# Optimization experiments

Hardware: AMD Instinct MI355X
Metric: run time of the kernel (lower is better)

## Reference

```python
import jax, jax.numpy as jnp
import numpy as np

N, E, MUL, ATTR, NBASIS = 30000, 480000, 32, 8, 8
AVG_NEIGH = 16.0
INV_SQRT3 = 1.0 / np.sqrt(3.0).astype(np.float32)  # wigner 3j (1,1,0)
LOG2 = float(np.log(2.0))


def ssp(x):
    # shifted softplus: softplus(x) - log(2)
    return jax.nn.softplus(x) - LOG2


def setup_inputs() -> dict:
    key = jax.random.key(0)
    ks = jax.random.split(key, 15)
    return {
        "node_s": jax.random.normal(ks[0], (N, MUL), jnp.float32),
        "node_v": jax.random.normal(ks[1], (N, MUL, 3), jnp.float32),
        "node_attr": jax.random.uniform(ks[2], (N, ATTR), jnp.float32),
        "edge_attr": jax.random.normal(ks[3], (E, 4), jnp.float32),       # [sh0 | sh1(3)]
        "edge_scalars": jax.random.uniform(ks[4], (E, NBASIS), jnp.float32),
        "W1_0": jax.random.normal(ks[5], (MUL, MUL), jnp.float32),
        "W1_1": jax.random.normal(ks[6], (MUL, MUL), jnp.float32),
        "Wfc1": jax.random.normal(ks[7], (NBASIS, NBASIS), jnp.float32),
        "Wfc2": jax.random.normal(ks[8], (NBASIS, 4 * MUL), jnp.float32),
        "W2_0": jax.random.normal(ks[9], (2 * MUL, MUL), jnp.float32),
        "W2_1": jax.random.normal(ks[10], (2 * MUL, MUL), jnp.float32),
        "Wsc0": jax.random.normal(ks[11], (MUL, ATTR, MUL), jnp.float32),
        "Wsc1": jax.random.normal(ks[12], (MUL, ATTR, MUL), jnp.float32),
        "edge_src": jax.random.randint(ks[13], (E,), 0, N, jnp.int32),
        "edge_dst": jax.random.randint(ks[14], (E,), 0, N, jnp.int32),
    }


def reference(node_s, node_v, node_attr, edge_attr, edge_scalars,
              W1_0, W1_1, Wfc1, Wfc2, W2_0, W2_1, Wsc0, Wsc1,
              edge_src, edge_dst):
    n_nodes, mul = node_s.shape
    # --- fc: radial MLP -> per-edge TP weights (shared_weights=False) ---
    h = ssp(edge_scalars @ Wfc1 * (1.0 / np.sqrt(Wfc1.shape[0])))
    w = h @ Wfc2 * (1.0 / np.sqrt(Wfc2.shape[0]))                 # [E, 4*MUL]
    w00, w01, w10, w11 = jnp.split(w, 4, axis=1)                  # instruction order
    # --- lin1: per-irrep linear (fan-in normalized) ---
    inv_m = 1.0 / np.sqrt(mul)
    x0 = node_s @ W1_0 * inv_m                                    # [N, MUL]
    x1 = jnp.einsum('nud,uw->nwd', node_v, W1_1) * inv_m          # [N, MUL, 3]
    # --- gather destination-node features per edge ---
    x0d, x1d = x0[edge_dst], x1[edge_dst]
    sh0, sh1 = edge_attr[:, :1], edge_attr[:, 1:4]
    # --- uvu tensor product with per-edge weights ---
    s_a = w00 * x0d * sh0                                         # 0e x 0e -> 0e
    s_b = w11 * jnp.einsum('eud,ed->eu', x1d, sh1) * INV_SQRT3    # 1o x 1o -> 0e
    v_a = (w01 * x0d)[:, :, None] * sh1[:, None, :]               # 0e x 1o -> 1o
    v_b = w10[:, :, None] * x1d * sh0[:, :, None]                 # 1o x 0e -> 1o
    mid_s = jnp.concatenate([s_a, s_b], axis=1)                   # [E, 64]  (64x0e)
    mid_v = jnp.concatenate([v_a, v_b], axis=1)                   # [E, 64, 3] (64x1o)
    # --- scatter-sum over edge_src, normalized by sqrt(avg_num_neighbors) ---
    inv_nb = 1.0 / np.sqrt(AVG_NEIGH)
    agg_s = jax.ops.segment_sum(mid_s, edge_src, num_segments=n_nodes) * inv_nb
    agg_v = jax.ops.segment_sum(mid_v, edge_src, num_segments=n_nodes) * inv_nb
    # --- lin2 ---
    inv_2m = 1.0 / np.sqrt(2.0 * mul)
    out0 = agg_s @ W2_0 * inv_2m                                  # [N, MUL]
    out1 = jnp.einsum('nud,uw->nwd', agg_v, W2_1) * inv_2m        # [N, MUL, 3]
    # --- self-connection: fully-connected TP (attr is scalar 8x0e) ---
    sc_norm = 1.0 / np.sqrt(mul * node_attr.shape[1])
    sc0 = jnp.einsum('nu,nv,uvw->nw', node_s, node_attr, Wsc0) * sc_norm
    sc1 = jnp.einsum('nud,nv,uvw->nwd', node_v, node_attr, Wsc1) * sc_norm
    o0 = out0 + sc0
    o1 = out1 + sc1
    return jnp.concatenate([o0, o1.reshape(n_nodes, mul * 3)], axis=1)  # [N, 128]
```

## Files before the change

### kernel.cpp

```cpp
#include <hip/hip_runtime.h>
#include <math.h>

#define N_NODES 30000
#define N_EDGES 480000

typedef __attribute__((ext_vector_type(8))) short short8;
typedef __attribute__((ext_vector_type(4))) float f32x4;
typedef __attribute__((ext_vector_type(2))) float f32x2;

__device__ __forceinline__ unsigned short f2bf(float f) {
    unsigned u = __float_as_uint(f);
    u += 0x7fff + ((u >> 16) & 1);
    return (unsigned short)(u >> 16);
}
__device__ __forceinline__ float bfLO(unsigned v) { return __uint_as_float(v << 16); }
__device__ __forceinline__ float bfHI(unsigned v) { return __uint_as_float(v & 0xffff0000u); }
__device__ __forceinline__ unsigned packbf(float a, float b) {
    return (unsigned)f2bf(a) | ((unsigned)f2bf(b) << 16);
}
__device__ __forceinline__ unsigned ptk(float a, float b) {
    return (__float_as_uint(a) >> 16) | (__float_as_uint(b) & 0xffff0000u);
}

union U8 { short8 v; unsigned u[4]; };
union C4 { f32x4 v; float f[4]; };

__global__ __launch_bounds__(256) void k_pre(
    const float* __restrict__ node_s,
    const float* __restrict__ node_v,
    const float* __restrict__ W1_0,
    const float* __restrict__ W1_1,
    const float* __restrict__ Wsc0,
    const float* __restrict__ Wsc1,
    const float* __restrict__ W2_0,
    const float* __restrict__ W2_1,
    const int* __restrict__ edge_src,
    int* __restrict__ deg,
    unsigned short* __restrict__ xnode,
    unsigned* __restrict__ bsc0,
    unsigned* __restrict__ bsc1,
    unsigned* __restrict__ b20,
    unsigned* __restrict__ b21)
{
    __shared__ float sVT[16 * 100];
    __shared__ float sXo[16 * 140];
    int tid = threadIdx.x;

    if (blockIdx.x >= 1875) {
        int b = blockIdx.x - 1875;
        const float* Wm = (b == 0) ? Wsc0 : (b == 1) ? Wsc1 : (b == 2) ? W2_0 : W2_1;
        unsigned* dst = (b == 0) ? bsc0 : (b == 1) ? bsc1 : (b == 2) ? b20 : b21;
        float scale = (b < 2) ? 0.0625f : 0.03125f;
        int nu = (b < 2) ? 4096 : 1024;
        for (int idx = tid; idx < nu; idx += 256) {
            int jp = idx & 3;
            int lane = (idx >> 2) & 63;
            int ft = (idx >> 8) & 1;
            int kc = idx >> 9;
            int quad = lane >> 4, col = lane & 15;
            int k = kc * 32 + quad * 8 + jp * 2;
            int c = ft * 16 + col;
            dst[idx] = packbf(Wm[k * 32 + c] * scale, Wm[(k + 1) * 32 + c] * scale);
        }
        return;
    }

    atomicAdd(&deg[edge_src[blockIdx.x * 256 + tid]], 1);

    int nbase = blockIdx.x * 16;
    for (int i = tid; i < 1536; i += 256) {
        int nl = i / 96, r = i - nl * 96;
        int u = r / 3, d = r - u * 3;
        sVT[nl * 100 + d * 32 + u] = node_v[(size_t)nbase * 96 + i];
    }
    __syncthreads();

    int lane = tid & 63;
    int wv = tid >> 6;
    int col = lane & 15, quad = lane >> 4, m = lane & 15;

    const float* W1 = (wv == 0) ? W1_0 : W1_1;
    U8 bf0, bf1;
#pragma unroll
    for (int p = 0; p < 4; ++p) {
        int k = quad * 8 + 2 * p;
        bf0.u[p] = packbf(W1[k * 32 + col],      W1[(k + 1) * 32 + col]);
        bf1.u[p] = packbf(W1[k * 32 + col + 16], W1[(k + 1) * 32 + col + 16]);
    }

    U8 af;
    if (wv == 0) {
        const float* sp = node_s + (size_t)(nbase + m) * 32 + quad * 8;
        float4 a0 = *(const float4*)(sp);
        float4 a1 = *(const float4*)(sp + 4);
        af.u[0] = packbf(a0.x, a0.y); af.u[1] = packbf(a0.z, a0.w);
        af.u[2] = packbf(a1.x, a1.y); af.u[3] = packbf(a1.z, a1.w);
    } else {
        int R = 16 * (wv - 1) + m;
        int nl = R / 3, d = R - nl * 3;
        const float* vp = sVT + nl * 100 + d * 32 + quad * 8;
        af.u[0] = packbf(vp[0], vp[1]); af.u[1] = packbf(vp[2], vp[3]);
        af.u[2] = packbf(vp[4], vp[5]); af.u[3] = packbf(vp[6], vp[7]);
    }

    f32x4 acc0 = {0.f, 0.f, 0.f, 0.f};
    f32x4 acc1 = {0.f, 0.f, 0.f, 0.f};
    acc0 = __builtin_amdgcn_mfma_f32_16x16x32_bf16(af.v, bf0.v, acc0, 0, 0, 0);
    acc1 = __builtin_amdgcn_mfma_f32_16x16x32_bf16(af.v, bf1.v, acc1, 0, 0, 0);

    C4 c0, c1;
    c0.v = acc0; c1.v = acc1;
    if (wv == 0) {
#pragma unroll
        for (int r = 0; r < 4; ++r) {
            int nl = (quad << 2) + r;
            sXo[nl * 140 + col]      = c0.f[r];
            sXo[nl * 140 + col + 16] = c1.f[r];
        }
    } else {
#pragma unroll
        for (int r = 0; r < 4; ++r) {
            int R = 16 * (wv - 1) + (quad << 2) + r;
            int nl = R / 3, d = R - nl * 3;
            sXo[nl * 140 + (1 + d) * 34 + col]      = c0.f[r];
            sXo[nl * 140 + (1 + d) * 34 + col + 16] = c1.f[r];
        }
    }
    __syncthreads();

    const float inv_m = 0.1767766953f;
    for (int i = tid; i < 512; i += 256) {
        int nl = i >> 5, u = i & 31;
        const float* xp = sXo + nl * 140;
        uint2 pk;
        pk.x = packbf(xp[u] * inv_m,       xp[34 + u] * inv_m);
        pk.y = packbf(xp[68 + u] * inv_m,  xp[102 + u] * inv_m);
        *(uint2*)(xnode + (size_t)(nbase + nl) * 128 + u * 4) = pk;
    }
}

__global__ __launch_bounds__(1024) void scan_kernel(const int* __restrict__ deg,
                                                    int* __restrict__ offs,
                                                    int* __restrict__ cursor) {
    __shared__ int sdeg[N_NODES];
    __shared__ int wsum[16];
    int tid = threadIdx.x;
#pragma unroll
    for (int k = 0; k < 30; ++k) {
        int idx = k * 1024 + tid;
        if (idx < N_NODES) sdeg[idx] = deg[idx];
    }
    __syncthreads();
    int base = tid * 30;
    int s = 0;
    if (base < N_NODES) {
#pragma unroll
        for (int k = 0; k < 30; ++k) s += sdeg[base + k];
    }
    int lane = tid & 63, wid = tid >> 6;
    int inc = s;
#pragma unroll
    for (int d = 1; d < 64; d <<= 1) {
        int o = __shfl_up(inc, d, 64);
        if (lane >= d) inc += o;
    }
    if (lane == 63) wsum[wid] = inc;
    __syncthreads();
    if (tid < 16) {
        int v = wsum[tid];
        int t = v;
#pragma unroll
        for (int d = 1; d < 16; d <<= 1) {
            int o = __shfl_up(t, d, 64);
            if (tid >= d) t += o;
        }
        wsum[tid] = t - v;
    }
    __syncthreads();
    int run = inc - s + wsum[wid];
    if (base < N_NODES) {
#pragma unroll
        for (int k = 0; k < 30; ++k) {
            int n = base + k;
            int d = sdeg[n];
            sdeg[n] = run;
            run += d;
        }
    }
    __syncthreads();
#pragma unroll
    for (int k = 0; k < 30; ++k) {
        int idx = k * 1024 + tid;
        if (idx < N_NODES) {
            int v = sdeg[idx];
            offs[idx] = v;
            cursor[idx] = v;
        }
    }
    if (tid == 0) offs[N_NODES] = N_EDGES;
}

__global__ __launch_bounds__(256) void fill_kernel(
    const float* __restrict__ edge_attr,
    const float* __restrict__ edge_scalars,
    const float* __restrict__ Wfc1,
    const int* __restrict__ edge_src,
    const int* __restrict__ edge_dst,
    int* __restrict__ cursor,
    uint4* __restrict__ rec)
{
    __shared__ float sW[64];
    int tid = threadIdx.x;
    if (tid < 64) sW[tid] = Wfc1[tid];
    __syncthreads();

    int e = blockIdx.x * 256 + tid;
    float4 es0 = *(const float4*)(edge_scalars + (size_t)e * 8);
    float4 es1 = *(const float4*)(edge_scalars + (size_t)e * 8 + 4);
    float4 ea  = *(const float4*)(edge_attr + (size_t)e * 4);
    int src = edge_src[e];
    int dst = edge_dst[e];
    int pos = atomicAdd(&cursor[src], 1);

    const float inv8 = 0.3535533906f;
    float h[8];
#pragma unroll
    for (int i = 0; i < 8; ++i) {
        float acc = es0.x * sW[0 * 8 + i];
        acc = fmaf(es0.y, sW[1 * 8 + i], acc);
        acc = fmaf(es0.z, sW[2 * 8 + i], acc);
        acc = fmaf(es0.w, sW[3 * 8 + i], acc);
        acc = fmaf(es1.x, sW[4 * 8 + i], acc);
        acc = fmaf(es1.y, sW[5 * 8 + i], acc);
        acc = fmaf(es1.z, sW[6 * 8 + i], acc);
        acc = fmaf(es1.w, sW[7 * 8 + i], acc);
        acc *= inv8;
        float ax = fabsf(acc);
        float tt = __expf(-ax);
        h[i] = fmaxf(acc, 0.f) + __logf(1.f + tt) - 0.6931471806f;
    }
    uint4 r0, r1;
    r0.x = packbf(h[0], h[1]); r0.y = packbf(h[2], h[3]);
    r0.z = packbf(h[4], h[5]); r0.w = packbf(h[6], h[7]);
    r1.x = packbf(ea.x, ea.y); r1.y = packbf(ea.z, ea.w);
    r1.z = (unsigned)dst; r1.w = 0;
    rec[2 * pos]     = r0;
    rec[2 * pos + 1] = r1;
}

__global__ __launch_bounds__(256) void k_main(
    const int* __restrict__ offs,
    const uint4* __restrict__ rec,
    const float* __restrict__ Wfc2,
    const unsigned short* __restrict__ xnode,
    const float* __restrict__ node_s,
    const float* __restrict__ node_v,
    const float* __restrict__ node_attr,
    const unsigned* __restrict__ bsc0,
    const unsigned* __restrict__ bsc1,
    const unsigned* __restrict__ b20,
    const unsigned* __restrict__ b21,
    float* __restrict__ out)
{
    __shared__ float sS[16 * 33];
    __shared__ float sV[16 * 100];
    __shared__ unsigned short sAgg[16 * 264];
    int tid = threadIdx.x;
    int lane = tid & 63;
    int u = lane & 31;
    int half = lane >> 5;
    int wv = tid >> 6;
    int nbase = blockIdx.x * 16;

    for (int i = tid; i < 512; i += 256)
        sS[(i >> 5) * 33 + (i & 31)] = node_s[(size_t)nbase * 32 + i];
    for (int i = tid; i < 1536; i += 256)
        sV[(i / 96) * 100 + (i % 96)] = node_v[(size_t)nbase * 96 + i];

    const float inv8 = 0.3535533906f;
    const float inv_s3 = 0.5773502692f;
    f32x2 wfA[8], wfB[8];
#pragma unroll
    for (int i = 0; i < 8; ++i) {
        wfA[i].x = Wfc2[i * 128 + u] * inv8;
        wfA[i].y = Wfc2[i * 128 + 32 + u] * inv8;
        wfB[i].x = Wfc2[i * 128 + 64 + u] * inv8;
        wfB[i].y = Wfc2[i * 128 + 96 + u] * inv8 * inv_s3;
    }

    for (int jn = 0; jn < 4; ++jn) {
        int nl = wv * 4 + jn;
        int node = nbase + nl;
        int beg = offs[node], end = offs[node + 1];
        float a_sa = 0.f, a_sb = 0.f;
        f32x2 a_va01 = {0.f, 0.f}, a_vb01 = {0.f, 0.f};
        float a_va2 = 0.f, a_vb2 = 0.f;

        if (end > beg) {
            int last = end - 1;
            int i = beg + half;
            int p = min(i, last);
            uint4 a0 = rec[2 * p], a1 = rec[2 * p + 1];
            p = min(i + 2, last);
            uint4 b0 = rec[2 * p], b1 = rec[2 * p + 1];
            p = min(i + 4, last);
            uint4 c0 = rec[2 * p], c1 = rec[2 * p + 1];
            uint2 xA = *(const uint2*)(xnode + (size_t)(int)a1.z * 128 + u * 4);
            uint2 xB = *(const uint2*)(xnode + (size_t)(int)b1.z * 128 + u * 4);

            for (; i < end; i += 2) {
                int pD = min(i + 6, last);
                uint4 d0 = rec[2 * pD], d1 = rec[2 * pD + 1];
                uint2 xC = *(const uint2*)(xnode + (size_t)(int)c1.z * 128 + u * 4);

                float hv[8];
                hv[0] = bfLO(a0.x); hv[1] = bfHI(a0.x);
                hv[2] = bfLO(a0.y); hv[3] = bfHI(a0.y);
                hv[4] = bfLO(a0.z); hv[5] = bfHI(a0.z);
                hv[6] = bfLO(a0.w); hv[7] = bfHI(a0.w);
                f32x2 aA = {0.f, 0.f}, aB = {0.f, 0.f};
#pragma unroll
                for (int q = 0; q < 8; ++q) {
                    f32x2 hh = {hv[q], hv[q]};
                    aA = __builtin_elementwise_fma(hh, wfA[q], aA);
                    aB = __builtin_elementwise_fma(hh, wfB[q], aB);
                }
                float a00 = aA.x, a01 = aA.y, a10 = aB.x, a11 = aB.y;

                float sh0 = bfLO(a1.x), s1xe = bfHI(a1.x);
                float s1ye = bfLO(a1.y), s1ze = bfHI(a1.y);
                float x0 = bfLO(xA.x), xd0 = bfHI(xA.x);
                float xd1 = bfLO(xA.y), xd2 = bfHI(xA.y);

                float dot = xd0 * s1xe + xd1 * s1ye + xd2 * s1ze;
                a_sa = fmaf(a00 * sh0, x0, a_sa);
                a_sb = fmaf(a11, dot, a_sb);
                float w01x0 = a01 * x0;
                float t10 = a10 * sh0;
                f32x2 wb = {w01x0, w01x0};
                f32x2 tb = {t10, t10};
                f32x2 s01 = {s1xe, s1ye};
                f32x2 xd01 = {xd0, xd1};
                a_va01 = __builtin_elementwise_fma(wb, s01, a_va01);
                a_vb01 = __builtin_elementwise_fma(tb, xd01, a_vb01);
                a_va2 = fmaf(w01x0, s1ze, a_va2);
                a_vb2 = fmaf(t10, xd2, a_vb2);

                a0 = b0; a1 = b1; xA = xB;
                b0 = c0; b1 = c1; xB = xC;
                c0 = d0; c1 = d1;
            }
        }
        a_sa    += __shfl_xor(a_sa, 32, 64);
        a_sb    += __shfl_xor(a_sb, 32, 64);
        a_va01.x += __shfl_xor(a_va01.x, 32, 64);
        a_va01.y += __shfl_xor(a_va01.y, 32, 64);
        a_vb01.x += __shfl_xor(a_vb01.x, 32, 64);
        a_vb01.y += __shfl_xor(a_vb01.y, 32, 64);
        a_va2   += __shfl_xor(a_va2, 32, 64);
        a_vb2   += __shfl_xor(a_vb2, 32, 64);

        unsigned short* ap = sAgg + nl * 264;
        if (half == 0) {
            ap[u]       = f2bf(a_sa);
            ap[32 + u]  = f2bf(a_sb);
            ap[64 + u]  = f2bf(a_va01.x);
            ap[96 + u]  = f2bf(a_vb01.x);
        } else {
            ap[128 + u] = f2bf(a_va01.y);
            ap[160 + u] = f2bf(a_vb01.y);
            ap[192 + u] = f2bf(a_va2);
            ap[224 + u] = f2bf(a_vb2);
        }
    }
    __syncthreads();

    int col = lane & 15;
    int quad = lane >> 4;
    int m = col;
    bool is_s = (wv == 0);
    int sub = wv - 1;

    const short* Bs = (const short*)(is_s ? bsc0 : bsc1);
    const short* B2 = (const short*)(is_s ? b20 : b21);

    int aBase, fbase, fstep, n_a;
    if (is_s) {
        aBase = m * 264;
        fbase = m * 33;
        fstep = 1;
        n_a = nbase + m;
    } else {
        int r16 = 16 * sub + m;
        int nl = r16 / 3;
        int dd = r16 - nl * 3;
        aBase = nl * 264 + 64 + 64 * dd;
        fbase = nl * 100 + dd;
        fstep = 3;
        n_a = nbase + nl;
    }
    float4 A0 = *(const float4*)(node_attr + (size_t)n_a * 8);
    float4 A1 = *(const float4*)(node_attr + (size_t)n_a * 8 + 4);
    float aa0 = A0.x, aa1 = A0.y, aa2 = A0.z, aa3 = A0.w;
    float aa4 = A1.x, aa5 = A1.y, aa6 = A1.z, aa7 = A1.w;

    f32x4 acc0 = {0.f, 0.f, 0.f, 0.f};
    f32x4 acc1 = {0.f, 0.f, 0.f, 0.f};

#pragma unroll
    for (int kc = 0; kc < 2; ++kc) {
        short8 af = *(const short8*)((const short*)sAgg + aBase + kc * 32 + quad * 8);
        short8 bf0 = *(const short8*)(B2 + ((kc * 2 + 0) * 64 + lane) * 8);
        short8 bf1 = *(const short8*)(B2 + ((kc * 2 + 1) * 64 + lane) * 8);
        acc0 = __builtin_amdgcn_mfma_f32_16x16x32_bf16(af, bf0, acc0, 0, 0, 0);
        acc1 = __builtin_amdgcn_mfma_f32_16x16x32_bf16(af, bf1, acc1, 0, 0, 0);
    }
    const float* Sf = is_s ? sS : sV;
#pragma unroll
    for (int kc = 0; kc < 8; ++kc) {
        int uu = kc * 4 + quad;
        float f = Sf[fbase + uu * fstep];
        U8 af;
        af.u[0] = ptk(f * aa0, f * aa1);
        af.u[1] = ptk(f * aa2, f * aa3);
        af.u[2] = ptk(f * aa4, f * aa5);
        af.u[3] = ptk(f * aa6, f * aa7);
        short8 bf0 = *(const short8*)(Bs + ((kc * 2 + 0) * 64 + lane) * 8);
        short8 bf1 = *(const short8*)(Bs + ((kc * 2 + 1) * 64 + lane) * 8);
        acc0 = __builtin_amdgcn_mfma_f32_16x16x32_bf16(af.v, bf0, acc0, 0, 0, 0);
        acc1 = __builtin_amdgcn_mfma_f32_16x16x32_bf16(af.v, bf1, acc1, 0, 0, 0);
    }

    C4 c0, c1;
    c0.v = acc0; c1.v = acc1;
    if (is_s) {
#pragma unroll
        for (int r = 0; r < 4; ++r) {
            int n = nbase + (quad << 2) + r;
            out[(size_t)n * 128 + col]      = c0.f[r];
            out[(size_t)n * 128 + col + 16] = c1.f[r];
        }
    } else {
#pragma unroll
        for (int r = 0; r < 4; ++r) {
            int rl = 16 * sub + (quad << 2) + r;
            int nn = rl / 3;
            int dd = rl - nn * 3;
            int n = nbase + nn;
            out[(size_t)n * 128 + 32 + 3 * col + dd]        = c0.f[r];
            out[(size_t)n * 128 + 32 + 3 * (col + 16) + dd] = c1.f[r];
        }
    }
}

extern "C" void kernel_launch(void* const* d_in, const int* in_sizes, int n_in,
                              void* d_out, int out_size, void* d_ws, size_t ws_size,
                              hipStream_t stream) {
    const float* node_s       = (const float*)d_in[0];
    const float* node_v       = (const float*)d_in[1];
    const float* node_attr    = (const float*)d_in[2];
    const float* edge_attr    = (const float*)d_in[3];
    const float* edge_scalars = (const float*)d_in[4];
    const float* W1_0 = (const float*)d_in[5];
    const float* W1_1 = (const float*)d_in[6];
    const float* Wfc1 = (const float*)d_in[7];
    const float* Wfc2 = (const float*)d_in[8];
    const float* W2_0 = (const float*)d_in[9];
    const float* W2_1 = (const float*)d_in[10];
    const float* Wsc0 = (const float*)d_in[11];
    const float* Wsc1 = (const float*)d_in[12];
    const int* edge_src = (const int*)d_in[13];
    const int* edge_dst = (const int*)d_in[14];

    char* ws = (char*)d_ws;
    unsigned short* xnode = (unsigned short*)(ws);
    uint4* rec            = (uint4*)(ws + 7680000);
    int* deg    = (int*)(ws + 23040000);
    int* offs   = (int*)(ws + 23160000);
    int* cursor = (int*)(ws + 23280016);
    unsigned* bsc0 = (unsigned*)(ws + 23400064);
    unsigned* bsc1 = (unsigned*)(ws + 23416448);
    unsigned* b20  = (unsigned*)(ws + 23432832);
    unsigned* b21  = (unsigned*)(ws + 23436928);

    hipMemsetAsync(deg, 0, (size_t)N_NODES * sizeof(int), stream);
    k_pre<<<1879, 256, 0, stream>>>(node_s, node_v, W1_0, W1_1, Wsc0, Wsc1,
                                    W2_0, W2_1, edge_src, deg, xnode,
                                    bsc0, bsc1, b20, b21);
    scan_kernel<<<1, 1024, 0, stream>>>(deg, offs, cursor);
    fill_kernel<<<1875, 256, 0, stream>>>(edge_attr, edge_scalars, Wfc1,
                                          edge_src, edge_dst, cursor, rec);
    k_main<<<1875, 256, 0, stream>>>(offs, rec, Wfc2, xnode,
                                     node_s, node_v, node_attr,
                                     bsc0, bsc1, b20, b21, (float*)d_out);
}
```

Before: 227.9 us.

## Split fused main kernel into per-node gather kernel and separate MFMA GEMM kernel

```diff
diff --git a/kernel.cpp b/kernel.cpp
--- a/kernel.cpp
+++ b/kernel.cpp
@@ -243,16 +243,161 @@
     r0.x = packbf(h[0], h[1]); r0.y = packbf(h[2], h[3]);
     r0.z = packbf(h[4], h[5]); r0.w = packbf(h[6], h[7]);
     r1.x = packbf(ea.x, ea.y); r1.y = packbf(ea.z, ea.w);
-    r1.z = (unsigned)dst; r1.w = 0;
+    r1.z = ((unsigned)dst) << 8;
+    r1.w = 0;
     rec[2 * pos]     = r0;
     rec[2 * pos + 1] = r1;
 }
 
-__global__ __launch_bounds__(256) void k_main(
+struct GAcc {
+    float sa, sb, va2, vb2;
+    f32x2 va01, vb01;
+};
+
+__device__ __forceinline__ void gstep(
+    uint4& RS0, uint4& RS1, uint2& XS, const uint4& RN1, uint2& XN,
+    int& t, int cntH, int& pf, int L,
+    const char* recc, const char* xbc,
+    const f32x2* wfA, const f32x2* wfB, GAcc& g)
+{
+    float hv[8];
+    hv[0] = bfLO(RS0.x); hv[1] = bfHI(RS0.x);
+    hv[2] = bfLO(RS0.y); hv[3] = bfHI(RS0.y);
+    hv[4] = bfLO(RS0.z); hv[5] = bfHI(RS0.z);
+    hv[6] = bfLO(RS0.w); hv[7] = bfHI(RS0.w);
+    float sh0  = bfLO(RS1.x), s1xe = bfHI(RS1.x);
+    float s1ye = bfLO(RS1.y), s1ze = bfHI(RS1.y);
+    float xv0 = bfLO(XS.x), xd0 = bfHI(XS.x);
+    float xd1 = bfLO(XS.y), xd2 = bfHI(XS.y);
+    bool ok = (t < cntH);
+
+    RS0 = *(const uint4*)(recc + pf);
+    RS1 = *(const uint4*)(recc + pf + 16);
+    pf = min(pf + 64, L);
+    XN = *(const uint2*)(xbc + RN1.z);
+
+    f32x2 aA = {0.f, 0.f}, aB = {0.f, 0.f};
+#pragma unroll
+    for (int q = 0; q < 8; ++q) {
+        f32x2 hh = {hv[q], hv[q]};
+        aA = __builtin_elementwise_fma(hh, wfA[q], aA);
+        aB = __builtin_elementwise_fma(hh, wfB[q], aB);
+    }
+    float a00 = ok ? aA.x : 0.f;
+    float a01 = ok ? aA.y : 0.f;
+    float a10 = ok ? aB.x : 0.f;
+    float a11 = ok ? aB.y : 0.f;
+
+    float dot = xd0 * s1xe + xd1 * s1ye + xd2 * s1ze;
+    g.sa = fmaf(a00 * sh0, xv0, g.sa);
+    g.sb = fmaf(a11, dot, g.sb);
+    float w01x0 = a01 * xv0;
+    float t10 = a10 * sh0;
+    f32x2 wb = {w01x0, w01x0};
+    f32x2 tb = {t10, t10};
+    f32x2 s01 = {s1xe, s1ye};
+    f32x2 xd01 = {xd0, xd1};
+    g.va01 = __builtin_elementwise_fma(wb, s01, g.va01);
+    g.vb01 = __builtin_elementwise_fma(tb, xd01, g.vb01);
+    g.va2 = fmaf(w01x0, s1ze, g.va2);
+    g.vb2 = fmaf(t10, xd2, g.vb2);
+    ++t;
+}
+
+__global__ __launch_bounds__(256, 5) void k_gather(
     const int* __restrict__ offs,
     const uint4* __restrict__ rec,
     const float* __restrict__ Wfc2,
     const unsigned short* __restrict__ xnode,
+    unsigned short* __restrict__ agg)
+{
+    __shared__ float sWf[1024];
+    int tid = threadIdx.x;
+    const float inv8 = 0.3535533906f;
+    const float inv_s3 = 0.5773502692f;
+    for (int i = tid; i < 1024; i += 256) {
+        float sc = ((i & 127) >= 96) ? inv8 * inv_s3 : inv8;
+        sWf[i] = Wfc2[i] * sc;
+    }
+    __syncthreads();
+
+    int lane = tid & 63;
+    int u = lane & 31;
+    int half = lane >> 5;
+    int wv = tid >> 6;
+    int node = blockIdx.x * 4 + wv;
+
+    f32x2 wfA[8], wfB[8];
+#pragma unroll
+    for (int q = 0; q < 8; ++q) {
+        const float* wp = sWf + q * 128 + u;
+        wfA[q].x = wp[0];  wfA[q].y = wp[32];
+        wfB[q].x = wp[64]; wfB[q].y = wp[96];
+    }
+
+    int beg = offs[node], end = offs[node + 1];
+    int cnt = end - beg;
+
+    GAcc g;
+    g.sa = 0.f; g.sb = 0.f; g.va2 = 0.f; g.vb2 = 0.f;
+    g.va01 = (f32x2){0.f, 0.f};
+    g.vb01 = (f32x2){0.f, 0.f};
+
+    if (cnt > 0) {
+        const char* recc = (const char*)rec;
+        const char* xbc  = (const char*)xnode + u * 8;
+        int T = (cnt + 1) >> 1;
+        int cntH = (cnt + 1 - half) >> 1;
+        int L = (end - 1) * 32;
+        int b0 = (beg + half) * 32;
+
+        uint4 r00, r01, r10, r11, r20, r21;
+        uint2 x0, x1, x2;
+        x2.x = 0u; x2.y = 0u;
+        int p;
+        p = min(b0, L);        r00 = *(const uint4*)(recc + p); r01 = *(const uint4*)(recc + p + 16);
+        p = min(b0 + 64, L);   r10 = *(const uint4*)(recc + p); r11 = *(const uint4*)(recc + p + 16);
+        p = min(b0 + 128, L);  r20 = *(const uint4*)(recc + p); r21 = *(const uint4*)(recc + p + 16);
+        int pf = min(b0 + 192, L);
+        x0 = *(const uint2*)(xbc + r01.z);
+        x1 = *(const uint2*)(xbc + r11.z);
+
+        int t = 0;
+        int Tm = T - 2;
+        while (t < Tm) {
+            gstep(r00, r01, x0, r21, x2, t, cntH, pf, L, recc, xbc, wfA, wfB, g);
+            gstep(r10, r11, x1, r01, x0, t, cntH, pf, L, recc, xbc, wfA, wfB, g);
+            gstep(r20, r21, x2, r11, x1, t, cntH, pf, L, recc, xbc, wfA, wfB, g);
+        }
+        if (t < T) gstep(r00, r01, x0, r21, x2, t, cntH, pf, L, recc, xbc, wfA, wfB, g);
+        if (t < T) gstep(r10, r11, x1, r01, x0, t, cntH, pf, L, recc, xbc, wfA, wfB, g);
+    }
+
+    g.sa      += __shfl_xor(g.sa, 32, 64);
+    g.sb      += __shfl_xor(g.sb, 32, 64);
+    g.va01.x  += __shfl_xor(g.va01.x, 32, 64);
+    g.va01.y  += __shfl_xor(g.va01.y, 32, 64);
+    g.vb01.x  += __shfl_xor(g.vb01.x, 32, 64);
+    g.vb01.y  += __shfl_xor(g.vb01.y, 32, 64);
+    g.va2     += __shfl_xor(g.va2, 32, 64);
+    g.vb2     += __shfl_xor(g.vb2, 32, 64);
+
+    unsigned short* ap = agg + (size_t)node * 256;
+    if (half == 0) {
+        ap[u]       = f2bf(g.sa);
+        ap[32 + u]  = f2bf(g.sb);
+        ap[64 + u]  = f2bf(g.va01.x);
+        ap[96 + u]  = f2bf(g.vb01.x);
+    } else {
+        ap[128 + u] = f2bf(g.va01.y);
+        ap[160 + u] = f2bf(g.vb01.y);
+        ap[192 + u] = f2bf(g.va2);
+        ap[224 + u] = f2bf(g.vb2);
+    }
+}
+
+__global__ __launch_bounds__(256) void k_gemm(
+    const unsigned short* agg,
     const float* __restrict__ node_s,
     const float* __restrict__ node_v,
     const float* __restrict__ node_attr,
@@ -260,15 +405,12 @@
     const unsigned* __restrict__ bsc1,
     const unsigned* __restrict__ b20,
     const unsigned* __restrict__ b21,
-    float* __restrict__ out)
+    float* out)
 {
     __shared__ float sS[16 * 33];
     __shared__ float sV[16 * 100];
-    __shared__ unsigned short sAgg[16 * 264];
     int tid = threadIdx.x;
     int lane = tid & 63;
-    int u = lane & 31;
-    int half = lane >> 5;
     int wv = tid >> 6;
     int nbase = blockIdx.x * 16;
 
@@ -276,104 +418,6 @@
         sS[(i >> 5) * 33 + (i & 31)] = node_s[(size_t)nbase * 32 + i];
     for (int i = tid; i < 1536; i += 256)
         sV[(i / 96) * 100 + (i % 96)] = node_v[(size_t)nbase * 96 + i];
-
-    const float inv8 = 0.3535533906f;
-    const float inv_s3 = 0.5773502692f;
-    f32x2 wfA[8], wfB[8];
-#pragma unroll
-    for (int i = 0; i < 8; ++i) {
-        wfA[i].x = Wfc2[i * 128 + u] * inv8;
-        wfA[i].y = Wfc2[i * 128 + 32 + u] * inv8;
-        wfB[i].x = Wfc2[i * 128 + 64 + u] * inv8;
-        wfB[i].y = Wfc2[i * 128 + 96 + u] * inv8 * inv_s3;
-    }
-
-    for (int jn = 0; jn < 4; ++jn) {
-        int nl = wv * 4 + jn;
-        int node = nbase + nl;
-        int beg = offs[node], end = offs[node + 1];
-        float a_sa = 0.f, a_sb = 0.f;
-        f32x2 a_va01 = {0.f, 0.f}, a_vb01 = {0.f, 0.f};
-        float a_va2 = 0.f, a_vb2 = 0.f;
-
-        if (end > beg) {
-            int last = end - 1;
-            int i = beg + half;
-            int p = min(i, last);
-            uint4 a0 = rec[2 * p], a1 = rec[2 * p + 1];
-            p = min(i + 2, last);
-            uint4 b0 = rec[2 * p], b1 = rec[2 * p + 1];
-            p = min(i + 4, last);
-            uint4 c0 = rec[2 * p], c1 = rec[2 * p + 1];
-            uint2 xA = *(const uint2*)(xnode + (size_t)(int)a1.z * 128 + u * 4);
-            uint2 xB = *(const uint2*)(xnode + (size_t)(int)b1.z * 128 + u * 4);
-
-            for (; i < end; i += 2) {
-                int pD = min(i + 6, last);
-                uint4 d0 = rec[2 * pD], d1 = rec[2 * pD + 1];
-                uint2 xC = *(const uint2*)(xnode + (size_t)(int)c1.z * 128 + u * 4);
-
-                float hv[8];
-                hv[0] = bfLO(a0.x); hv[1] = bfHI(a0.x);
-                hv[2] = bfLO(a0.y); hv[3] = bfHI(a0.y);
-                hv[4] = bfLO(a0.z); hv[5] = bfHI(a0.z);
-                hv[6] = bfLO(a0.w); hv[7] = bfHI(a0.w);
-                f32x2 aA = {0.f, 0.f}, aB = {0.f, 0.f};
-#pragma unroll
-                for (int q = 0; q < 8; ++q) {
-                    f32x2 hh = {hv[q], hv[q]};
-                    aA = __builtin_elementwise_fma(hh, wfA[q], aA);
-                    aB = __builtin_elementwise_fma(hh, wfB[q], aB);
-                }
-                float a00 = aA.x, a01 = aA.y, a10 = aB.x, a11 = aB.y;
-
-                float sh0 = bfLO(a1.x), s1xe = bfHI(a1.x);
-                float s1ye = bfLO(a1.y), s1ze = bfHI(a1.y);
-                float x0 = bfLO(xA.x), xd0 = bfHI(xA.x);
-                float xd1 = bfLO(xA.y), xd2 = bfHI(xA.y);
-
-                float dot = xd0 * s1xe + xd1 * s1ye + xd2 * s1ze;
-                a_sa = fmaf(a00 * sh0, x0, a_sa);
-                a_sb = fmaf(a11, dot, a_sb);
-                float w01x0 = a01 * x0;
-                float t10 = a10 * sh0;
-                f32x2 wb = {w01x0, w01x0};
-                f32x2 tb = {t10, t10};
-                f32x2 s01 = {s1xe, s1ye};
-                f32x2 xd01 = {xd0, xd1};
-                a_va01 = __builtin_elementwise_fma(wb, s01, a_va01);
-                a_vb01 = __builtin_elementwise_fma(tb, xd01, a_vb01);
-                a_va2 = fmaf(w01x0, s1ze, a_va2);
-                a_vb2 = fmaf(t10, xd2, a_vb2);
-
-                a0 = b0; a1 = b1; xA = xB;
-                b0 = c0; b1 = c1; xB = xC;
-                c0 = d0; c1 = d1;
-            }
-        }
-        a_sa    += __shfl_xor(a_sa, 32, 64);
-        a_sb    += __shfl_xor(a_sb, 32, 64);
-        a_va01.x += __shfl_xor(a_va01.x, 32, 64);
-        a_va01.y += __shfl_xor(a_va01.y, 32, 64);
-        a_vb01.x += __shfl_xor(a_vb01.x, 32, 64);
-        a_vb01.y += __shfl_xor(a_vb01.y, 32, 64);
-        a_va2   += __shfl_xor(a_va2, 32, 64);
-        a_vb2   += __shfl_xor(a_vb2, 32, 64);
-
-        unsigned short* ap = sAgg + nl * 264;
-        if (half == 0) {
-            ap[u]       = f2bf(a_sa);
-            ap[32 + u]  = f2bf(a_sb);
-            ap[64 + u]  = f2bf(a_va01.x);
-            ap[96 + u]  = f2bf(a_vb01.x);
-        } else {
-            ap[128 + u] = f2bf(a_va01.y);
-            ap[160 + u] = f2bf(a_vb01.y);
-            ap[192 + u] = f2bf(a_va2);
-            ap[224 + u] = f2bf(a_vb2);
-        }
-    }
-    __syncthreads();
 
     int col = lane & 15;
     int quad = lane >> 4;
@@ -386,7 +430,7 @@
 
     int aBase, fbase, fstep, n_a;
     if (is_s) {
-        aBase = m * 264;
+        aBase = m * 256;
         fbase = m * 33;
         fstep = 1;
         n_a = nbase + m;
@@ -394,27 +438,37 @@
         int r16 = 16 * sub + m;
         int nl = r16 / 3;
         int dd = r16 - nl * 3;
-        aBase = nl * 264 + 64 + 64 * dd;
+        aBase = nl * 256 + 64 + 64 * dd;
         fbase = nl * 100 + dd;
         fstep = 3;
         n_a = nbase + nl;
     }
+
+    const short* aggp = (const short*)agg + (size_t)nbase * 256 + aBase + quad * 8;
+    short8 afW0 = *(const short8*)(aggp);
+    short8 afW1 = *(const short8*)(aggp + 32);
+
     float4 A0 = *(const float4*)(node_attr + (size_t)n_a * 8);
     float4 A1 = *(const float4*)(node_attr + (size_t)n_a * 8 + 4);
     float aa0 = A0.x, aa1 = A0.y, aa2 = A0.z, aa3 = A0.w;
     float aa4 = A1.x, aa5 = A1.y, aa6 = A1.z, aa7 = A1.w;
 
+    __syncthreads();
+
     f32x4 acc0 = {0.f, 0.f, 0.f, 0.f};
     f32x4 acc1 = {0.f, 0.f, 0.f, 0.f};
 
-#pragma unroll
-    for (int kc = 0; kc < 2; ++kc) {
-        short8 af = *(const short8*)((const short*)sAgg + aBase + kc * 32 + quad * 8);
-        short8 bf0 = *(const short8*)(B2 + ((kc * 2 + 0) * 64 + lane) * 8);
-        short8 bf1 = *(const short8*)(B2 + ((kc * 2 + 1) * 64 + lane) * 8);
-        acc0 = __builtin_amdgcn_mfma_f32_16x16x32_bf16(af, bf0, acc0, 0, 0, 0);
-        acc1 = __builtin_amdgcn_mfma_f32_16x16x32_bf16(af, bf1, acc1, 0, 0, 0);
-    }
+    {
+        short8 bf0 = *(const short8*)(B2 + (0 * 64 + lane) * 8);
+        short8 bf1 = *(const short8*)(B2 + (1 * 64 + lane) * 8);
+        acc0 = __builtin_amdgcn_mfma_f32_16x16x32_bf16(afW0, bf0, acc0, 0, 0, 0);
+        acc1 = __builtin_amdgcn_mfma_f32_16x16x32_bf16(afW0, bf1, acc1, 0, 0, 0);
+        bf0 = *(const short8*)(B2 + (2 * 64 + lane) * 8);
+        bf1 = *(const short8*)(B2 + (3 * 64 + lane) * 8);
+        acc0 = __builtin_amdgcn_mfma_f32_16x16x32_bf16(afW1, bf0, acc0, 0, 0, 0);
+        acc1 = __builtin_amdgcn_mfma_f32_16x16x32_bf16(afW1, bf1, acc1, 0, 0, 0);
+    }
+
     const float* Sf = is_s ? sS : sV;
 #pragma unroll
     for (int kc = 0; kc < 8; ++kc) {
@@ -490,7 +544,9 @@
     scan_kernel<<<1, 1024, 0, stream>>>(deg, offs, cursor);
     fill_kernel<<<1875, 256, 0, stream>>>(edge_attr, edge_scalars, Wfc1,
                                           edge_src, edge_dst, cursor, rec);
-    k_main<<<1875, 256, 0, stream>>>(offs, rec, Wfc2, xnode,
+    k_gather<<<7500, 256, 0, stream>>>(offs, rec, Wfc2, xnode,
+                                       (unsigned short*)d_out);
+    k_gemm<<<1875, 256, 0, stream>>>((const unsigned short*)d_out,
                                      node_s, node_v, node_attr,
                                      bsc0, bsc1, b20, b21, (float*)d_out);
 }
```

After: 238.3 us. 1.05x slower.
